# Kernel tuning notes

Measured on AMD Instinct MI355X. Metric: run time of the kernel, lower is better.

Reference implementation:

```python
import jax, jax.numpy as jnp
import numpy as np

N = 100000      # nodes
E = 800000      # edges (before self-loops)
F_IN = 128      # num_features
HID = 64        # hidden_dim
HEADS = 4       # gat1 heads


def setup_inputs() -> dict:
    key = jax.random.key(0)
    ks = jax.random.split(key, 24)
    s = 0.05
    d = {}
    d["x"] = jax.random.normal(ks[0], (N, F_IN), jnp.float32)
    d["edge_index"] = jax.random.randint(ks[1], (2, E), 0, N, dtype=jnp.int32)
    # GATConv 1: in=128 -> out=64 per head, 4 heads, concat
    d["W1"] = jax.random.normal(ks[2], (F_IN, HEADS * HID), jnp.float32) * s
    d["att_src1"] = jax.random.normal(ks[3], (HEADS, HID), jnp.float32) * s
    d["att_dst1"] = jax.random.normal(ks[4], (HEADS, HID), jnp.float32) * s
    d["b1"] = jnp.zeros((HEADS * HID,), jnp.float32)
    # GATConv 2: in=256 -> out=64, 1 head
    d["W2"] = jax.random.normal(ks[5], (HEADS * HID, HID), jnp.float32) * s
    d["att_src2"] = jax.random.normal(ks[6], (1, HID), jnp.float32) * s
    d["att_dst2"] = jax.random.normal(ks[7], (1, HID), jnp.float32) * s
    d["b2"] = jnp.zeros((HID,), jnp.float32)
    # 2-layer GRU (input 64, hidden 64), h0 = 0
    for l in range(2):
        d[f"gru_Wih{l}"] = jax.random.normal(ks[8 + 4 * l], (3 * HID, HID), jnp.float32) * s
        d[f"gru_Whh{l}"] = jax.random.normal(ks[9 + 4 * l], (3 * HID, HID), jnp.float32) * s
        d[f"gru_bih{l}"] = jnp.zeros((3 * HID,), jnp.float32)
        d[f"gru_bhh{l}"] = jnp.zeros((3 * HID,), jnp.float32)
    d["fc_W"] = jax.random.normal(ks[16], (3, HID), jnp.float32) * s
    d["fc_b"] = jnp.zeros((3,), jnp.float32)
    return d


def gat_conv(x, edge_index, W, att_src, att_dst, bias, heads):
    """PyG GATConv (eval mode, add_self_loops=True): gather -> LeakyReLU ->
    segment softmax over destination nodes -> scatter-add, heads concatenated."""
    n = x.shape[0]
    loops = jnp.arange(n, dtype=edge_index.dtype)
    src = jnp.concatenate([edge_index[0], loops])
    dst = jnp.concatenate([edge_index[1], loops])
    h = (x @ W).reshape(n, heads, -1)                       # [N,H,C]
    a_src = jnp.sum(h * att_src, axis=-1)                    # [N,H]
    a_dst = jnp.sum(h * att_dst, axis=-1)                    # [N,H]
    e = jax.nn.leaky_relu(a_src[src] + a_dst[dst], 0.2)      # [Et,H]
    m = jax.ops.segment_max(e, dst, num_segments=n)          # stable softmax max
    p = jnp.exp(e - m[dst])
    denom = jax.ops.segment_sum(p, dst, num_segments=n)
    alpha = p / (denom[dst] + 1e-16)                         # [Et,H]
    out = jax.ops.segment_sum(h[src] * alpha[:, :, None], dst, num_segments=n)
    return out.reshape(n, -1) + bias                         # concat heads


def gru_cell_zero_h(x, Wih, Whh, bih, bhh):
    """One GRU step with h_prev = 0 (seq_len == 1, batch_first)."""
    h0 = jnp.zeros_like(x)
    gi = x @ Wih.T + bih
    gh = h0 @ Whh.T + bhh
    i_r, i_z, i_n = jnp.split(gi, 3, axis=-1)
    h_r, h_z, h_n = jnp.split(gh, 3, axis=-1)
    r = jax.nn.sigmoid(i_r + h_r)
    z = jax.nn.sigmoid(i_z + h_z)
    nnew = jnp.tanh(i_n + r * h_n)
    return (1.0 - z) * nnew + z * h0


def reference(x, edge_index, W1, att_src1, att_dst1, b1, W2, att_src2, att_dst2, b2,
              gru_Wih0, gru_Whh0, gru_bih0, gru_bhh0,
              gru_Wih1, gru_Whh1, gru_bih1, gru_bhh1, fc_W, fc_b):
    x1 = jax.nn.relu(gat_conv(x, edge_index, W1, att_src1, att_dst1, b1, HEADS))
    # dropout p=0.2 is identity in eval mode
    x2 = gat_conv(x1, edge_index, W2, att_src2, att_dst2, b2, 1)
    h = gru_cell_zero_h(x2, gru_Wih0, gru_Whh0, gru_bih0, gru_bhh0)
    h = gru_cell_zero_h(h, gru_Wih1, gru_Whh1, gru_bih1, gru_bhh1)
    return h @ fc_W.T + fc_b
```

## Files before the change

### kernel.cpp

```cpp
#include <hip/hip_runtime.h>
#include <math.h>

#define N_FIN 128
#define C1    256
#define NH    4
#define HD    64
#define G3    192

typedef _Float16 f16x8 __attribute__((ext_vector_type(8)));
typedef float    f32x4 __attribute__((ext_vector_type(4)));

static __device__ __forceinline__ float lrelu(float x) { return x >= 0.0f ? x : 0.2f * x; }
static __device__ __forceinline__ float sigm(float x)  { return 1.0f / (1.0f + __expf(-x)); }

static __device__ __forceinline__ float bf2f(unsigned int u)
{
    union { unsigned int i; float f; } c; c.i = u << 16; return c.f;
}
static __device__ __forceinline__ unsigned short f2bf(float f)
{
    union { float f; unsigned int i; } c; c.f = f;
    unsigned int i = c.i + 0x7FFFu + ((c.i >> 16) & 1u);
    return (unsigned short)(i >> 16);
}

__global__ __launch_bounds__(256) void k_deg_init(int n, int* __restrict__ deg)
{
    int i = blockIdx.x * blockDim.x + threadIdx.x;
    if (i < n) deg[i] = 1;
}

__global__ __launch_bounds__(256) void k_hist(int E, const int* __restrict__ edst, int* __restrict__ deg)
{
    int e = blockIdx.x * blockDim.x + threadIdx.x;
    if (e < E) atomicAdd(&deg[edst[e]], 1);
}

__global__ __launch_bounds__(1024) void k_scan_block(int n, const int* __restrict__ deg,
                                                     int* __restrict__ incl, int* __restrict__ bsum)
{
    __shared__ int sh[1024];
    int t = threadIdx.x;
    int i = blockIdx.x * 1024 + t;
    sh[t] = (i < n) ? deg[i] : 0;
    __syncthreads();
    #pragma unroll
    for (int off = 1; off < 1024; off <<= 1) {
        int u = (t >= off) ? sh[t - off] : 0;
        __syncthreads();
        sh[t] += u;
        __syncthreads();
    }
    if (i < n) incl[i] = sh[t];
    if (t == 1023) bsum[blockIdx.x] = sh[1023];
}

__global__ void k_scan_bsum(int nb, int* __restrict__ bsum)
{
    if (threadIdx.x == 0 && blockIdx.x == 0) {
        int run = 0;
        for (int b = 0; b < nb; ++b) { int v = bsum[b]; bsum[b] = run; run += v; }
    }
}

__global__ __launch_bounds__(256) void k_rowptr(int n, const int* __restrict__ incl,
                                                const int* __restrict__ bsum, int* __restrict__ rowptr)
{
    int i = blockIdx.x * blockDim.x + threadIdx.x;
    if (i < n) rowptr[i + 1] = incl[i] + bsum[i >> 10];
    if (i == 0) rowptr[0] = 0;
}

__global__ __launch_bounds__(256) void k_cursor(int n, const int* __restrict__ rowptr, int* __restrict__ cursor)
{
    int i = blockIdx.x * blockDim.x + threadIdx.x;
    if (i < n) cursor[i] = rowptr[i];
}

__global__ __launch_bounds__(256) void k_fill(int E, int n, const int* __restrict__ esrc,
                                              const int* __restrict__ edst,
                                              int* __restrict__ cursor, int* __restrict__ col)
{
    int t = blockIdx.x * blockDim.x + threadIdx.x;
    if (t < E) {
        int p = atomicAdd(&cursor[edst[t]], 1);
        col[p] = esrc[t];
    } else if (t < E + n) {
        int v = t - E;
        int p = atomicAdd(&cursor[v], 1);
        col[p] = v;
    }
}

template<int BN, bool AHALF>
__global__ __launch_bounds__(256) void gemm_mfma(int M, int K,
    const void* __restrict__ Ap, int lda, const float* __restrict__ B, int ldb,
    unsigned short* __restrict__ C, int ldc)
{
    __shared__ _Float16 Al[128][40];
    __shared__ _Float16 Bt[BN][40];
    const int tid = threadIdx.x;
    const int wid = tid >> 6, l = tid & 63;
    const int l15 = l & 15, lk = (l >> 4) * 8;
    const int row0 = blockIdx.x * 128, col0 = blockIdx.y * BN;

    f32x4 acc[2][BN / 16];
    #pragma unroll
    for (int rf = 0; rf < 2; ++rf)
        #pragma unroll
        for (int cf = 0; cf < BN / 16; ++cf)
            acc[rf][cf] = (f32x4){0.f, 0.f, 0.f, 0.f};

    for (int k0 = 0; k0 < K; k0 += 32) {
        if (AHALF) {
            const _Float16* A = (const _Float16*)Ap;
            #pragma unroll
            for (int u = 0; u < 2; ++u) {
                int i = tid + u * 256;
                int r = i >> 2, kq = (i & 3) * 8;
                int ar = row0 + r; ar = ar < M ? ar : M - 1;
                *(f16x8*)&Al[r][kq] = *(const f16x8*)(A + (size_t)ar * lda + k0 + kq);
            }
        } else {
            const float* A = (const float*)Ap;
            #pragma unroll
            for (int u = 0; u < 4; ++u) {
                int i = tid + u * 256;
                int r = i >> 3, kq = (i & 7) * 4;
                int ar = row0 + r; ar = ar < M ? ar : M - 1;
                float4 v = *(const float4*)(A + (size_t)ar * lda + k0 + kq);
                Al[r][kq + 0] = (_Float16)v.x; Al[r][kq + 1] = (_Float16)v.y;
                Al[r][kq + 2] = (_Float16)v.z; Al[r][kq + 3] = (_Float16)v.w;
            }
        }
        {
            constexpr int GK  = 256 / BN;
            constexpr int KPG = 32 / GK;
            int n = tid % BN, kh = tid / BN;
            #pragma unroll
            for (int g = 0; g < KPG / 8; ++g) {
                f16x8 t;
                #pragma unroll
                for (int kk = 0; kk < 8; ++kk)
                    t[kk] = (_Float16)B[(size_t)(k0 + kh * KPG + g * 8 + kk) * ldb + col0 + n];
                *(f16x8*)&Bt[n][kh * KPG + g * 8] = t;
            }
        }
        __syncthreads();
        f16x8 a0 = *(const f16x8*)&Al[wid * 32 + l15][lk];
        f16x8 a1 = *(const f16x8*)&Al[wid * 32 + 16 + l15][lk];
        #pragma unroll
        for (int cf = 0; cf < BN / 16; ++cf) {
            f16x8 b = *(const f16x8*)&Bt[cf * 16 + l15][lk];
            acc[0][cf] = __builtin_amdgcn_mfma_f32_16x16x32_f16(a0, b, acc[0][cf], 0, 0, 0);
            acc[1][cf] = __builtin_amdgcn_mfma_f32_16x16x32_f16(a1, b, acc[1][cf], 0, 0, 0);
        }
        __syncthreads();
    }
    #pragma unroll
    for (int rf = 0; rf < 2; ++rf)
        #pragma unroll
        for (int i = 0; i < 4; ++i) {
            int r = row0 + wid * 32 + rf * 16 + (l >> 4) * 4 + i;
            if (r < M) {
                #pragma unroll
                for (int cf = 0; cf < BN / 16; ++cf)
                    C[(size_t)r * ldc + col0 + cf * 16 + l15] = f2bf(acc[rf][cf][i]);
            }
        }
}

__global__ __launch_bounds__(256) void k_gru_mfma(int M,
    const _Float16* __restrict__ A,
    const float* __restrict__ Wih,
    const float* __restrict__ bih, const float* __restrict__ bhh,
    _Float16* __restrict__ hout)
{
    __shared__ _Float16 Al[128][72];
    __shared__ _Float16 Bt[192][72];
    const int tid = threadIdx.x, wid = tid >> 6, l = tid & 63;
    const int l15 = l & 15, lk = (l >> 4) * 8;
    const int row0 = blockIdx.x * 128;

    f32x4 acc[2][12];
    #pragma unroll
    for (int rf = 0; rf < 2; ++rf)
        #pragma unroll
        for (int cf = 0; cf < 12; ++cf)
            acc[rf][cf] = (f32x4){0.f, 0.f, 0.f, 0.f};

    #pragma unroll
    for (int u = 0; u < 4; ++u) {
        int i = tid + u * 256;
        int r = i >> 3, kq = (i & 7) * 8;
        int ar = row0 + r; ar = ar < M ? ar : M - 1;
        *(f16x8*)&Al[r][kq] = *(const f16x8*)(A + (size_t)ar * 64 + kq);
    }
    if (tid < 192) {
        #pragma unroll
        for (int kq = 0; kq < 64; kq += 4) {
            float4 v = *(const float4*)(Wih + (size_t)tid * 64 + kq);
            Bt[tid][kq + 0] = (_Float16)v.x; Bt[tid][kq + 1] = (_Float16)v.y;
            Bt[tid][kq + 2] = (_Float16)v.z; Bt[tid][kq + 3] = (_Float16)v.w;
        }
    }
    __syncthreads();
    #pragma unroll
    for (int ks = 0; ks < 2; ++ks) {
        f16x8 a0 = *(const f16x8*)&Al[wid * 32 + l15][ks * 32 + lk];
        f16x8 a1 = *(const f16x8*)&Al[wid * 32 + 16 + l15][ks * 32 + lk];
        #pragma unroll
        for (int cf = 0; cf < 12; ++cf) {
            f16x8 b = *(const f16x8*)&Bt[cf * 16 + l15][ks * 32 + lk];
            acc[0][cf] = __builtin_amdgcn_mfma_f32_16x16x32_f16(a0, b, acc[0][cf], 0, 0, 0);
            acc[1][cf] = __builtin_amdgcn_mfma_f32_16x16x32_f16(a1, b, acc[1][cf], 0, 0, 0);
        }
    }
    #pragma unroll
    for (int rf = 0; rf < 2; ++rf)
        #pragma unroll
        for (int i = 0; i < 4; ++i) {
            int r = row0 + wid * 32 + rf * 16 + (l >> 4) * 4 + i;
            if (r < M) {
                #pragma unroll
                for (int cf = 0; cf < 4; ++cf) {
                    int u = cf * 16 + l15;
                    float gr = acc[rf][cf][i]     + bih[u]       + bhh[u];
                    float gz = acc[rf][cf + 4][i] + bih[64 + u]  + bhh[64 + u];
                    float rr = sigm(gr), zz = sigm(gz);
                    float nn = tanhf(acc[rf][cf + 8][i] + bih[128 + u] + rr * bhh[128 + u]);
                    hout[(size_t)r * 64 + u] = (_Float16)((1.0f - zz) * nn);
                }
            }
        }
}

__global__ __launch_bounds__(256) void k_att1(int n, const unsigned short* __restrict__ h1b,
    const float* __restrict__ att_src, const float* __restrict__ att_dst,
    float* __restrict__ a_src, float* __restrict__ a_dst)
{
    int v = (blockIdx.x * blockDim.x + threadIdx.x) >> 6;
    int lane = threadIdx.x & 63;
    if (v >= n) return;
    const unsigned short* hr = h1b + (size_t)v * C1;
    #pragma unroll
    for (int h = 0; h < NH; ++h) {
        float x = bf2f(hr[h * HD + lane]);
        float ps = x * att_src[h * HD + lane];
        float pd = x * att_dst[h * HD + lane];
        #pragma unroll
        for (int off = 32; off > 0; off >>= 1) {
            ps += __shfl_down(ps, off);
            pd += __shfl_down(pd, off);
        }
        if (lane == 0) { a_src[v * NH + h] = ps; a_dst[v * NH + h] = pd; }
    }
}

__global__ __launch_bounds__(256) void k_att2(int n, const unsigned short* __restrict__ h2b,
    const float* __restrict__ att_src, const float* __restrict__ att_dst,
    float* __restrict__ a_src, float* __restrict__ a_dst)
{
    int v = (blockIdx.x * blockDim.x + threadIdx.x) >> 6;
    int lane = threadIdx.x & 63;
    if (v >= n) return;
    float x = bf2f(h2b[(size_t)v * HD + lane]);
    float ps = x * att_src[lane];
    float pd = x * att_dst[lane];
    #pragma unroll
    for (int off = 32; off > 0; off >>= 1) {
        ps += __shfl_down(ps, off);
        pd += __shfl_down(pd, off);
    }
    if (lane == 0) { a_src[v] = ps; a_dst[v] = pd; }
}

__global__ __launch_bounds__(256) void k_aggr1(int n, const int* __restrict__ rowptr,
    const int* __restrict__ col, const unsigned short* __restrict__ h1b,
    const float* __restrict__ a_src, const float* __restrict__ a_dst,
    const float* __restrict__ b1, _Float16* __restrict__ x1h)
{
    int v = (blockIdx.x * blockDim.x + threadIdx.x) >> 6;
    int lane = threadIdx.x & 63;
    if (v >= n) return;
    const int sub = lane >> 4;
    const int l   = lane & 15;
    int beg = rowptr[v], end = rowptr[v + 1];
    float ad = a_dst[(size_t)v * NH + sub];

    float sum = 0.0f;
    float4 acc = make_float4(0.f, 0.f, 0.f, 0.f);
    int i = beg;
    for (; i + 1 < end; i += 2) {
        int sA = col[i], sB = col[i + 1];
        float aA = a_src[(size_t)sA * NH + sub];
        float aB = a_src[(size_t)sB * NH + sub];
        uint2 uA = *reinterpret_cast<const uint2*>(h1b + (size_t)sA * C1 + sub * HD + l * 4);
        uint2 uB = *reinterpret_cast<const uint2*>(h1b + (size_t)sB * C1 + sub * HD + l * 4);
        float pA = __expf(fminf(lrelu(aA + ad), 50.f));
        float pB = __expf(fminf(lrelu(aB + ad), 50.f));
        sum += pA + pB;
        acc.x += pA * bf2f(uA.x & 0xffffu) + pB * bf2f(uB.x & 0xffffu);
        acc.y += pA * bf2f(uA.x >> 16)     + pB * bf2f(uB.x >> 16);
        acc.z += pA * bf2f(uA.y & 0xffffu) + pB * bf2f(uB.y & 0xffffu);
        acc.w += pA * bf2f(uA.y >> 16)     + pB * bf2f(uB.y >> 16);
    }
    if (i < end) {
        int s = col[i];
        float as = a_src[(size_t)s * NH + sub];
        uint2 u = *reinterpret_cast<const uint2*>(h1b + (size_t)s * C1 + sub * HD + l * 4);
        float p = __expf(fminf(lrelu(as + ad), 50.f));
        sum += p;
        acc.x += p * bf2f(u.x & 0xffffu);
        acc.y += p * bf2f(u.x >> 16);
        acc.z += p * bf2f(u.y & 0xffffu);
        acc.w += p * bf2f(u.y >> 16);
    }
    float inv = 1.0f / (sum + 1e-16f);
    float4 bb = *reinterpret_cast<const float4*>(b1 + sub * HD + l * 4);
    float rx = acc.x * inv + bb.x, ry = acc.y * inv + bb.y;
    float rz = acc.z * inv + bb.z, rw = acc.w * inv + bb.w;
    _Float16 o[4];
    o[0] = (_Float16)(rx > 0.f ? rx : 0.f);
    o[1] = (_Float16)(ry > 0.f ? ry : 0.f);
    o[2] = (_Float16)(rz > 0.f ? rz : 0.f);
    o[3] = (_Float16)(rw > 0.f ? rw : 0.f);
    *reinterpret_cast<uint2*>(x1h + (size_t)v * C1 + sub * HD + l * 4) = *reinterpret_cast<uint2*>(o);
}

__global__ __launch_bounds__(256) void k_aggr2(int n, const int* __restrict__ rowptr,
    const int* __restrict__ col, const unsigned short* __restrict__ h2b,
    const float* __restrict__ a_src, const float* __restrict__ a_dst,
    const float* __restrict__ b2, _Float16* __restrict__ x2h)
{
    int v = (blockIdx.x * blockDim.x + threadIdx.x) >> 6;
    int lane = threadIdx.x & 63;
    if (v >= n) return;
    const int sub = lane >> 4;
    const int l   = lane & 15;
    int beg = rowptr[v], end = rowptr[v + 1];
    float ad = a_dst[v];

    float sum = 0.0f;
    float4 acc = make_float4(0.f, 0.f, 0.f, 0.f);
    for (int i = beg + sub; i < end; i += 4) {
        int s = col[i];
        float p = __expf(fminf(lrelu(a_src[s] + ad), 50.f));
        sum += p;
        uint2 u = *reinterpret_cast<const uint2*>(h2b + (size_t)s * HD + l * 4);
        acc.x += p * bf2f(u.x & 0xffffu);
        acc.y += p * bf2f(u.x >> 16);
        acc.z += p * bf2f(u.y & 0xffffu);
        acc.w += p * bf2f(u.y >> 16);
    }
    sum += __shfl_xor(sum, 16); sum += __shfl_xor(sum, 32);
    acc.x += __shfl_xor(acc.x, 16); acc.x += __shfl_xor(acc.x, 32);
    acc.y += __shfl_xor(acc.y, 16); acc.y += __shfl_xor(acc.y, 32);
    acc.z += __shfl_xor(acc.z, 16); acc.z += __shfl_xor(acc.z, 32);
    acc.w += __shfl_xor(acc.w, 16); acc.w += __shfl_xor(acc.w, 32);

    if (sub == 0) {
        float inv = 1.0f / (sum + 1e-16f);
        float4 bb = *reinterpret_cast<const float4*>(b2 + l * 4);
        _Float16 o[4];
        o[0] = (_Float16)(acc.x * inv + bb.x);
        o[1] = (_Float16)(acc.y * inv + bb.y);
        o[2] = (_Float16)(acc.z * inv + bb.z);
        o[3] = (_Float16)(acc.w * inv + bb.w);
        *reinterpret_cast<uint2*>(x2h + (size_t)v * HD + l * 4) = *reinterpret_cast<uint2*>(o);
    }
}

__global__ __launch_bounds__(256) void k_fc(int n, const _Float16* __restrict__ h,
    const float* __restrict__ fcW, const float* __restrict__ fcb, float* __restrict__ out)
{
    int v = (blockIdx.x * blockDim.x + threadIdx.x) >> 6;
    int lane = threadIdx.x & 63;
    if (v >= n) return;
    float x = (float)h[(size_t)v * HD + lane];
    float p0 = x * fcW[lane];
    float p1 = x * fcW[64 + lane];
    float p2 = x * fcW[128 + lane];
    #pragma unroll
    for (int off = 32; off > 0; off >>= 1) {
        p0 += __shfl_down(p0, off);
        p1 += __shfl_down(p1, off);
        p2 += __shfl_down(p2, off);
    }
    if (lane == 0) {
        out[(size_t)v * 3 + 0] = p0 + fcb[0];
        out[(size_t)v * 3 + 1] = p1 + fcb[1];
        out[(size_t)v * 3 + 2] = p2 + fcb[2];
    }
}

extern "C" void kernel_launch(void* const* d_in, const int* in_sizes, int n_in,
                              void* d_out, int out_size, void* d_ws, size_t ws_size,
                              hipStream_t stream)
{
    const float* x    = (const float*)d_in[0];
    const int*   eidx = (const int*)d_in[1];
    const float* W1   = (const float*)d_in[2];
    const float* aS1  = (const float*)d_in[3];
    const float* aD1  = (const float*)d_in[4];
    const float* b1   = (const float*)d_in[5];
    const float* W2   = (const float*)d_in[6];
    const float* aS2  = (const float*)d_in[7];
    const float* aD2  = (const float*)d_in[8];
    const float* b2   = (const float*)d_in[9];
    const float* Wih0 = (const float*)d_in[10];
    const float* bih0 = (const float*)d_in[12];
    const float* bhh0 = (const float*)d_in[13];
    const float* Wih1 = (const float*)d_in[14];
    const float* bih1 = (const float*)d_in[16];
    const float* bhh1 = (const float*)d_in[17];
    const float* fcW  = (const float*)d_in[18];
    const float* fcb  = (const float*)d_in[19];
    float* out = (float*)d_out;

    const int N = in_sizes[0] / N_FIN;
    const int E = in_sizes[1] / 2;
    const int* esrc = eidx;
    const int* edst = eidx + E;

    float* f = (float*)d_ws;
    unsigned short* h1b = (unsigned short*)f;
    _Float16* hg  = (_Float16*)f;
    _Float16* x1h = (_Float16*)(f + (size_t)N * C1);
    float* g2s = f + 2 * (size_t)N * C1;
    unsigned short* g2b = (unsigned short*)g2s;
    float* x2s = g2s + (size_t)N * HD;
    _Float16* x2h = (_Float16*)x2s;
    _Float16* hg2 = (_Float16*)x2s;
    float* as1 = x2s + (size_t)N * HD;
    float* ad1 = as1 + (size_t)N * NH;
    float* as2 = ad1 + (size_t)N * NH;
    float* ad2 = as2 + (size_t)N;
    int* ip     = (int*)(ad2 + N);
    int* deg    = ip;
    int* rowptr = deg + N;
    int* cursor = rowptr + N + 1;
    int* incl   = cursor + N;
    int* bsum   = incl + N;
    int* col    = bsum + 256;

    const int nbN   = (N + 255) / 256;
    const int nbE   = (E + 255) / 256;
    const int nbEN  = (E + N + 255) / 256;
    const int nbW   = (N + 3) / 4;
    const int NB    = (N + 1023) / 1024;
    const int gM    = (N + 127) / 128;

    k_deg_init<<<nbN, 256, 0, stream>>>(N, deg);
    k_hist<<<nbE, 256, 0, stream>>>(E, edst, deg);
    k_scan_block<<<NB, 1024, 0, stream>>>(N, deg, incl, bsum);
    k_scan_bsum<<<1, 64, 0, stream>>>(NB, bsum);
    k_rowptr<<<nbN, 256, 0, stream>>>(N, incl, bsum, rowptr);
    k_cursor<<<nbN, 256, 0, stream>>>(N, rowptr, cursor);
    k_fill<<<nbEN, 256, 0, stream>>>(E, N, esrc, edst, cursor, col);

    gemm_mfma<128, false><<<dim3(gM, 2), 256, 0, stream>>>(N, N_FIN, x, N_FIN, W1, C1, h1b, C1);
    k_att1<<<nbW, 256, 0, stream>>>(N, h1b, aS1, aD1, as1, ad1);
    k_aggr1<<<nbW, 256, 0, stream>>>(N, rowptr, col, h1b, as1, ad1, b1, x1h);

    gemm_mfma<64, true><<<dim3(gM, 1), 256, 0, stream>>>(N, C1, x1h, C1, W2, HD, g2b, HD);
    k_att2<<<nbW, 256, 0, stream>>>(N, g2b, aS2, aD2, as2, ad2);
    k_aggr2<<<nbW, 256, 0, stream>>>(N, rowptr, col, g2b, as2, ad2, b2, x2h);

    k_gru_mfma<<<gM, 256, 0, stream>>>(N, x2h, Wih0, bih0, bhh0, hg);
    k_gru_mfma<<<gM, 256, 0, stream>>>(N, hg,  Wih1, bih1, bhh1, hg2);

    k_fc<<<nbW, 256, 0, stream>>>(N, hg2, fcW, fcb, out);

    (void)n_in; (void)out_size; (void)ws_size;
}
```

Baseline: 553.3 us.

## Fuse attention scores into GEMM epilogues and FC into GRU epilogue

```diff
diff --git a/kernel.cpp b/kernel.cpp
--- a/kernel.cpp
+++ b/kernel.cpp
@@ -5,7 +5,6 @@
 #define C1    256
 #define NH    4
 #define HD    64
-#define G3    192
 
 typedef _Float16 f16x8 __attribute__((ext_vector_type(8)));
 typedef float    f32x4 __attribute__((ext_vector_type(4)));
@@ -22,12 +21,6 @@
     union { float f; unsigned int i; } c; c.f = f;
     unsigned int i = c.i + 0x7FFFu + ((c.i >> 16) & 1u);
     return (unsigned short)(i >> 16);
-}
-
-__global__ __launch_bounds__(256) void k_deg_init(int n, int* __restrict__ deg)
-{
-    int i = blockIdx.x * blockDim.x + threadIdx.x;
-    if (i < n) deg[i] = 1;
 }
 
 __global__ __launch_bounds__(256) void k_hist(int E, const int* __restrict__ edst, int* __restrict__ deg)
@@ -64,17 +57,16 @@
 }
 
 __global__ __launch_bounds__(256) void k_rowptr(int n, const int* __restrict__ incl,
-                                                const int* __restrict__ bsum, int* __restrict__ rowptr)
+                                                const int* __restrict__ bsum,
+                                                int* __restrict__ rowptr, int* __restrict__ cursor)
 {
     int i = blockIdx.x * blockDim.x + threadIdx.x;
-    if (i < n) rowptr[i + 1] = incl[i] + bsum[i >> 10];
-    if (i == 0) rowptr[0] = 0;
-}
-
-__global__ __launch_bounds__(256) void k_cursor(int n, const int* __restrict__ rowptr, int* __restrict__ cursor)
-{
-    int i = blockIdx.x * blockDim.x + threadIdx.x;
-    if (i < n) cursor[i] = rowptr[i];
+    if (i < n) {
+        int v = incl[i] + bsum[i >> 10] + (i + 1);
+        rowptr[i + 1] = v;
+        if (i + 1 < n) cursor[i + 1] = v;
+        if (i == 0) { rowptr[0] = 0; cursor[0] = 0; }
+    }
 }
 
 __global__ __launch_bounds__(256) void k_fill(int E, int n, const int* __restrict__ esrc,
@@ -92,17 +84,19 @@
     }
 }
 
-template<int BN, bool AHALF>
+template<int BN, int NHEADS, bool AHALF>
 __global__ __launch_bounds__(256) void gemm_mfma(int M, int K,
     const void* __restrict__ Ap, int lda, const float* __restrict__ B, int ldb,
-    unsigned short* __restrict__ C, int ldc)
+    unsigned short* __restrict__ C, int ldc,
+    const float* __restrict__ att_src, const float* __restrict__ att_dst,
+    float* __restrict__ a_src, float* __restrict__ a_dst)
 {
     __shared__ _Float16 Al[128][40];
     __shared__ _Float16 Bt[BN][40];
     const int tid = threadIdx.x;
     const int wid = tid >> 6, l = tid & 63;
     const int l15 = l & 15, lk = (l >> 4) * 8;
-    const int row0 = blockIdx.x * 128, col0 = blockIdx.y * BN;
+    const int row0 = blockIdx.x * 128;
 
     f32x4 acc[2][BN / 16];
     #pragma unroll
@@ -142,7 +136,7 @@
                 f16x8 t;
                 #pragma unroll
                 for (int kk = 0; kk < 8; ++kk)
-                    t[kk] = (_Float16)B[(size_t)(k0 + kh * KPG + g * 8 + kk) * ldb + col0 + n];
+                    t[kk] = (_Float16)B[(size_t)(k0 + kh * KPG + g * 8 + kk) * ldb + n];
                 *(f16x8*)&Bt[n][kh * KPG + g * 8] = t;
             }
         }
@@ -157,24 +151,53 @@
         }
         __syncthreads();
     }
+    float asv[BN / 16], adv[BN / 16];
+    #pragma unroll
+    for (int cf = 0; cf < BN / 16; ++cf) {
+        int c = cf * 16 + l15;
+        asv[cf] = att_src[c]; adv[cf] = att_dst[c];
+    }
     #pragma unroll
     for (int rf = 0; rf < 2; ++rf)
         #pragma unroll
         for (int i = 0; i < 4; ++i) {
             int r = row0 + wid * 32 + rf * 16 + (l >> 4) * 4 + i;
-            if (r < M) {
+            bool ok = r < M;
+            if (ok) {
                 #pragma unroll
                 for (int cf = 0; cf < BN / 16; ++cf)
-                    C[(size_t)r * ldc + col0 + cf * 16 + l15] = f2bf(acc[rf][cf][i]);
-            }
-        }
-}
-
+                    C[(size_t)r * ldc + cf * 16 + l15] = f2bf(acc[rf][cf][i]);
+            }
+            #pragma unroll
+            for (int h = 0; h < NHEADS; ++h) {
+                float ps = 0.f, pd = 0.f;
+                #pragma unroll
+                for (int k = 0; k < 4; ++k) {
+                    int cf = h * 4 + k;
+                    ps += acc[rf][cf][i] * asv[cf];
+                    pd += acc[rf][cf][i] * adv[cf];
+                }
+                #pragma unroll
+                for (int m = 1; m < 16; m <<= 1) {
+                    ps += __shfl_xor(ps, m);
+                    pd += __shfl_xor(pd, m);
+                }
+                if (ok && l15 == 0) {
+                    a_src[(size_t)r * NHEADS + h] = ps;
+                    a_dst[(size_t)r * NHEADS + h] = pd;
+                }
+            }
+        }
+}
+
+template<bool FUSE_FC>
 __global__ __launch_bounds__(256) void k_gru_mfma(int M,
     const _Float16* __restrict__ A,
     const float* __restrict__ Wih,
     const float* __restrict__ bih, const float* __restrict__ bhh,
-    _Float16* __restrict__ hout)
+    _Float16* __restrict__ hout,
+    const float* __restrict__ fcW, const float* __restrict__ fcb,
+    float* __restrict__ out)
 {
     __shared__ _Float16 Al[128][72];
     __shared__ _Float16 Bt[192][72];
@@ -216,63 +239,49 @@
             acc[1][cf] = __builtin_amdgcn_mfma_f32_16x16x32_f16(a1, b, acc[1][cf], 0, 0, 0);
         }
     }
+    float fw[3][4];
+    if (FUSE_FC) {
+        #pragma unroll
+        for (int j = 0; j < 3; ++j)
+            #pragma unroll
+            for (int cf = 0; cf < 4; ++cf)
+                fw[j][cf] = fcW[j * 64 + cf * 16 + l15];
+    }
     #pragma unroll
     for (int rf = 0; rf < 2; ++rf)
         #pragma unroll
         for (int i = 0; i < 4; ++i) {
             int r = row0 + wid * 32 + rf * 16 + (l >> 4) * 4 + i;
-            if (r < M) {
+            bool ok = r < M;
+            float p0 = 0.f, p1 = 0.f, p2 = 0.f;
+            #pragma unroll
+            for (int cf = 0; cf < 4; ++cf) {
+                int u = cf * 16 + l15;
+                float gr = acc[rf][cf][i]     + bih[u]       + bhh[u];
+                float gz = acc[rf][cf + 4][i] + bih[64 + u]  + bhh[64 + u];
+                float rr = sigm(gr), zz = sigm(gz);
+                float nn = tanhf(acc[rf][cf + 8][i] + bih[128 + u] + rr * bhh[128 + u]);
+                float hv = (1.0f - zz) * nn;
+                if (!FUSE_FC) {
+                    if (ok) hout[(size_t)r * 64 + u] = (_Float16)hv;
+                } else {
+                    p0 += hv * fw[0][cf]; p1 += hv * fw[1][cf]; p2 += hv * fw[2][cf];
+                }
+            }
+            if (FUSE_FC) {
                 #pragma unroll
-                for (int cf = 0; cf < 4; ++cf) {
-                    int u = cf * 16 + l15;
-                    float gr = acc[rf][cf][i]     + bih[u]       + bhh[u];
-                    float gz = acc[rf][cf + 4][i] + bih[64 + u]  + bhh[64 + u];
-                    float rr = sigm(gr), zz = sigm(gz);
-                    float nn = tanhf(acc[rf][cf + 8][i] + bih[128 + u] + rr * bhh[128 + u]);
-                    hout[(size_t)r * 64 + u] = (_Float16)((1.0f - zz) * nn);
-                }
-            }
-        }
-}
-
-__global__ __launch_bounds__(256) void k_att1(int n, const unsigned short* __restrict__ h1b,
-    const float* __restrict__ att_src, const float* __restrict__ att_dst,
-    float* __restrict__ a_src, float* __restrict__ a_dst)
-{
-    int v = (blockIdx.x * blockDim.x + threadIdx.x) >> 6;
-    int lane = threadIdx.x & 63;
-    if (v >= n) return;
-    const unsigned short* hr = h1b + (size_t)v * C1;
-    #pragma unroll
-    for (int h = 0; h < NH; ++h) {
-        float x = bf2f(hr[h * HD + lane]);
-        float ps = x * att_src[h * HD + lane];
-        float pd = x * att_dst[h * HD + lane];
-        #pragma unroll
-        for (int off = 32; off > 0; off >>= 1) {
-            ps += __shfl_down(ps, off);
-            pd += __shfl_down(pd, off);
-        }
-        if (lane == 0) { a_src[v * NH + h] = ps; a_dst[v * NH + h] = pd; }
-    }
-}
-
-__global__ __launch_bounds__(256) void k_att2(int n, const unsigned short* __restrict__ h2b,
-    const float* __restrict__ att_src, const float* __restrict__ att_dst,
-    float* __restrict__ a_src, float* __restrict__ a_dst)
-{
-    int v = (blockIdx.x * blockDim.x + threadIdx.x) >> 6;
-    int lane = threadIdx.x & 63;
-    if (v >= n) return;
-    float x = bf2f(h2b[(size_t)v * HD + lane]);
-    float ps = x * att_src[lane];
-    float pd = x * att_dst[lane];
-    #pragma unroll
-    for (int off = 32; off > 0; off >>= 1) {
-        ps += __shfl_down(ps, off);
-        pd += __shfl_down(pd, off);
-    }
-    if (lane == 0) { a_src[v] = ps; a_dst[v] = pd; }
+                for (int m = 1; m < 16; m <<= 1) {
+                    p0 += __shfl_xor(p0, m);
+                    p1 += __shfl_xor(p1, m);
+                    p2 += __shfl_xor(p2, m);
+                }
+                if (ok && l15 == 0) {
+                    out[(size_t)r * 3 + 0] = p0 + fcb[0];
+                    out[(size_t)r * 3 + 1] = p1 + fcb[1];
+                    out[(size_t)r * 3 + 2] = p2 + fcb[2];
+                }
+            }
+        }
 }
 
 __global__ __launch_bounds__(256) void k_aggr1(int n, const int* __restrict__ rowptr,
@@ -291,21 +300,31 @@
     float sum = 0.0f;
     float4 acc = make_float4(0.f, 0.f, 0.f, 0.f);
     int i = beg;
-    for (; i + 1 < end; i += 2) {
-        int sA = col[i], sB = col[i + 1];
-        float aA = a_src[(size_t)sA * NH + sub];
-        float aB = a_src[(size_t)sB * NH + sub];
-        uint2 uA = *reinterpret_cast<const uint2*>(h1b + (size_t)sA * C1 + sub * HD + l * 4);
-        uint2 uB = *reinterpret_cast<const uint2*>(h1b + (size_t)sB * C1 + sub * HD + l * 4);
-        float pA = __expf(fminf(lrelu(aA + ad), 50.f));
-        float pB = __expf(fminf(lrelu(aB + ad), 50.f));
-        sum += pA + pB;
-        acc.x += pA * bf2f(uA.x & 0xffffu) + pB * bf2f(uB.x & 0xffffu);
-        acc.y += pA * bf2f(uA.x >> 16)     + pB * bf2f(uB.x >> 16);
-        acc.z += pA * bf2f(uA.y & 0xffffu) + pB * bf2f(uB.y & 0xffffu);
-        acc.w += pA * bf2f(uA.y >> 16)     + pB * bf2f(uB.y >> 16);
-    }
-    if (i < end) {
+    for (; i + 3 < end; i += 4) {
+        int s0 = col[i], s1 = col[i + 1], s2 = col[i + 2], s3 = col[i + 3];
+        float a0 = a_src[(size_t)s0 * NH + sub];
+        float a1 = a_src[(size_t)s1 * NH + sub];
+        float a2 = a_src[(size_t)s2 * NH + sub];
+        float a3 = a_src[(size_t)s3 * NH + sub];
+        uint2 u0 = *reinterpret_cast<const uint2*>(h1b + (size_t)s0 * C1 + sub * HD + l * 4);
+        uint2 u1 = *reinterpret_cast<const uint2*>(h1b + (size_t)s1 * C1 + sub * HD + l * 4);
+        uint2 u2 = *reinterpret_cast<const uint2*>(h1b + (size_t)s2 * C1 + sub * HD + l * 4);
+        uint2 u3 = *reinterpret_cast<const uint2*>(h1b + (size_t)s3 * C1 + sub * HD + l * 4);
+        float p0 = __expf(fminf(lrelu(a0 + ad), 50.f));
+        float p1 = __expf(fminf(lrelu(a1 + ad), 50.f));
+        float p2 = __expf(fminf(lrelu(a2 + ad), 50.f));
+        float p3 = __expf(fminf(lrelu(a3 + ad), 50.f));
+        sum += (p0 + p1) + (p2 + p3);
+        acc.x += p0 * bf2f(u0.x & 0xffffu) + p1 * bf2f(u1.x & 0xffffu)
+               + p2 * bf2f(u2.x & 0xffffu) + p3 * bf2f(u3.x & 0xffffu);
+        acc.y += p0 * bf2f(u0.x >> 16) + p1 * bf2f(u1.x >> 16)
+               + p2 * bf2f(u2.x >> 16) + p3 * bf2f(u3.x >> 16);
+        acc.z += p0 * bf2f(u0.y & 0xffffu) + p1 * bf2f(u1.y & 0xffffu)
+               + p2 * bf2f(u2.y & 0xffffu) + p3 * bf2f(u3.y & 0xffffu);
+        acc.w += p0 * bf2f(u0.y >> 16) + p1 * bf2f(u1.y >> 16)
+               + p2 * bf2f(u2.y >> 16) + p3 * bf2f(u3.y >> 16);
+    }
+    for (; i < end; ++i) {
         int s = col[i];
         float as = a_src[(size_t)s * NH + sub];
         uint2 u = *reinterpret_cast<const uint2*>(h1b + (size_t)s * C1 + sub * HD + l * 4);
@@ -368,29 +387,6 @@
         o[2] = (_Float16)(acc.z * inv + bb.z);
         o[3] = (_Float16)(acc.w * inv + bb.w);
         *reinterpret_cast<uint2*>(x2h + (size_t)v * HD + l * 4) = *reinterpret_cast<uint2*>(o);
-    }
-}
-
-__global__ __launch_bounds__(256) void k_fc(int n, const _Float16* __restrict__ h,
-    const float* __restrict__ fcW, const float* __restrict__ fcb, float* __restrict__ out)
-{
-    int v = (blockIdx.x * blockDim.x + threadIdx.x) >> 6;
-    int lane = threadIdx.x & 63;
-    if (v >= n) return;
-    float x = (float)h[(size_t)v * HD + lane];
-    float p0 = x * fcW[lane];
-    float p1 = x * fcW[64 + lane];
-    float p2 = x * fcW[128 + lane];
-    #pragma unroll
-    for (int off = 32; off > 0; off >>= 1) {
-        p0 += __shfl_down(p0, off);
-        p1 += __shfl_down(p1, off);
-        p2 += __shfl_down(p2, off);
-    }
-    if (lane == 0) {
-        out[(size_t)v * 3 + 0] = p0 + fcb[0];
-        out[(size_t)v * 3 + 1] = p1 + fcb[1];
-        out[(size_t)v * 3 + 2] = p2 + fcb[2];
     }
 }
 
@@ -431,7 +427,6 @@
     unsigned short* g2b = (unsigned short*)g2s;
     float* x2s = g2s + (size_t)N * HD;
     _Float16* x2h = (_Float16*)x2s;
-    _Float16* hg2 = (_Float16*)x2s;
     float* as1 = x2s + (size_t)N * HD;
     float* ad1 = as1 + (size_t)N * NH;
     float* as2 = ad1 + (size_t)N * NH;
@@ -451,26 +446,25 @@
     const int NB    = (N + 1023) / 1024;
     const int gM    = (N + 127) / 128;
 
-    k_deg_init<<<nbN, 256, 0, stream>>>(N, deg);
+    hipMemsetAsync(deg, 0, (size_t)N * sizeof(int), stream);
     k_hist<<<nbE, 256, 0, stream>>>(E, edst, deg);
     k_scan_block<<<NB, 1024, 0, stream>>>(N, deg, incl, bsum);
     k_scan_bsum<<<1, 64, 0, stream>>>(NB, bsum);
-    k_rowptr<<<nbN, 256, 0, stream>>>(N, incl, bsum, rowptr);
-    k_cursor<<<nbN, 256, 0, stream>>>(N, rowptr, cursor);
+    k_rowptr<<<nbN, 256, 0, stream>>>(N, incl, bsum, rowptr, cursor);
     k_fill<<<nbEN, 256, 0, stream>>>(E, N, esrc, edst, cursor, col);
 
-    gemm_mfma<128, false><<<dim3(gM, 2), 256, 0, stream>>>(N, N_FIN, x, N_FIN, W1, C1, h1b, C1);
-    k_att1<<<nbW, 256, 0, stream>>>(N, h1b, aS1, aD1, as1, ad1);
+    gemm_mfma<256, 4, false><<<gM, 256, 0, stream>>>(
+        N, N_FIN, x, N_FIN, W1, C1, h1b, C1, aS1, aD1, as1, ad1);
     k_aggr1<<<nbW, 256, 0, stream>>>(N, rowptr, col, h1b, as1, ad1, b1, x1h);
 
-    gemm_mfma<64, true><<<dim3(gM, 1), 256, 0, stream>>>(N, C1, x1h, C1, W2, HD, g2b, HD);
-    k_att2<<<nbW, 256, 0, stream>>>(N, g2b, aS2, aD2, as2, ad2);
+    gemm_mfma<64, 1, true><<<gM, 256, 0, stream>>>(
+        N, C1, x1h, C1, W2, HD, g2b, HD, aS2, aD2, as2, ad2);
     k_aggr2<<<nbW, 256, 0, stream>>>(N, rowptr, col, g2b, as2, ad2, b2, x2h);
 
-    k_gru_mfma<<<gM, 256, 0, stream>>>(N, x2h, Wih0, bih0, bhh0, hg);
-    k_gru_mfma<<<gM, 256, 0, stream>>>(N, hg,  Wih1, bih1, bhh1, hg2);
-
-    k_fc<<<nbW, 256, 0, stream>>>(N, hg2, fcW, fcb, out);
+    k_gru_mfma<false><<<gM, 256, 0, stream>>>(N, x2h, Wih0, bih0, bhh0, hg,
+                                              nullptr, nullptr, nullptr);
+    k_gru_mfma<true><<<gM, 256, 0, stream>>>(N, hg, Wih1, bih1, bhh1, nullptr,
+                                             fcW, fcb, out);
 
     (void)n_in; (void)out_size; (void)ws_size;
 }
```

Result: faster. 493.0 us (-10.9%).
